# Kernel tuning notes

Measured on AMD Instinct MI355X. Metric: run time of the kernel, lower is better.

The kernel has to match this reference:

```python
import jax, jax.numpy as jnp
import numpy as np
import math

B, S, D, H, DFF = 2, 2048, 1024, 16, 4096
DK = D // H
EPS = 1e-6


def setup_inputs() -> dict:
    key = jax.random.key(0)
    ks = jax.random.split(key, 12)
    s = 0.02
    return {
        "x": jax.random.normal(ks[0], (B, S, D), jnp.float32),
        "mask": jnp.ones((B, S), jnp.int32),
        "wq": jax.random.normal(ks[1], (D, D), jnp.float32) * s,
        "bq": jnp.zeros((D,), jnp.float32),
        "wk": jax.random.normal(ks[2], (D, D), jnp.float32) * s,
        "bk": jnp.zeros((D,), jnp.float32),
        "wv": jax.random.normal(ks[3], (D, D), jnp.float32) * s,
        "bv": jnp.zeros((D,), jnp.float32),
        "wo": jax.random.normal(ks[4], (D, D), jnp.float32) * s,
        "bo": jnp.zeros((D,), jnp.float32),
        "g1": jnp.ones((D,), jnp.float32),
        "b1": jnp.zeros((D,), jnp.float32),
        "g2": jnp.ones((D,), jnp.float32),
        "b2": jnp.zeros((D,), jnp.float32),
        "w1": jax.random.normal(ks[5], (DFF, D), jnp.float32) * s,
        "bf1": jnp.zeros((DFF,), jnp.float32),
        "w2": jax.random.normal(ks[6], (D, DFF), jnp.float32) * s,
        "bf2": jnp.zeros((D,), jnp.float32),
    }


def _gelu(x):
    # x * 0.5 * (1 + erf(x / sqrt(2))) -- exact erf-based GELU as in source
    return x * 0.5 * (1.0 + jax.lax.erf(x * (1.0 / math.sqrt(2.0))))


def _layernorm(x, gamma, beta):
    # torch.std uses unbiased (ddof=1); eps is OUTSIDE the sqrt in the source
    mean = jnp.mean(x, axis=-1, keepdims=True)
    std = jnp.std(x, axis=-1, keepdims=True, ddof=1)
    return gamma * (x - mean) / (std + EPS) + beta


def _block(x, mask, wq, bq, wk, bk, wv, bv, wo, bo, g1, b1, g2, b2, w1, bf1, w2, bf2):
    # multi-head attention (dropout is identity in eval mode)
    q = (x @ wq.T + bq).reshape(B, S, H, DK).transpose(0, 2, 1, 3)  # bhsd
    k = (x @ wk.T + bk).reshape(B, S, H, DK).transpose(0, 2, 1, 3)
    v = (x @ wv.T + bv).reshape(B, S, H, DK).transpose(0, 2, 1, 3)
    scores = jnp.einsum("bhsd,bhtd->bhst", q, k) / math.sqrt(DK)
    scores = jnp.where(mask[:, None, None, :] == 0, -1e9, scores)
    attn = jax.nn.softmax(scores, axis=-1)
    cv = jnp.einsum("bhst,bhtd->bhsd", attn, v)
    cv = cv.transpose(0, 2, 1, 3).reshape(B, S, D)
    hd = cv @ wo.T + bo
    # residual + norm1
    hd = _layernorm(x + hd, g1, b1)
    # position-wise FFN with erf GELU
    ff = _gelu(hd @ w1.T + bf1) @ w2.T + bf2
    return _layernorm(hd + ff, g2, b2)


def reference(x, mask, wq, bq, wk, bk, wv, bv, wo, bo, g1, b1, g2, b2, w1, bf1, w2, bf2):
    return _block(x, mask, wq, bq, wk, bk, wv, bv, wo, bo, g1, b1, g2, b2, w1, bf1, w2, bf2)
```

## Files before the change

kernel.cpp:

```cpp
#include <hip/hip_runtime.h>
#include <hip/hip_bf16.h>

#define B_   2
#define S_   2048
#define D_   1024
#define H_   16
#define DK_  64
#define DFF_ 4096
#define M_   (B_*S_)

typedef unsigned short u16;
typedef __attribute__((ext_vector_type(8))) short short8;
typedef __attribute__((ext_vector_type(4))) short bf16x4;
typedef __attribute__((ext_vector_type(4))) float floatx4;

__device__ __forceinline__ u16 f2bf(float f) {
    union { float f; unsigned u; } v; v.f = f;
    unsigned r = v.u + 0x7fffu + ((v.u >> 16) & 1u);
    return (u16)(r >> 16);
}
__device__ __forceinline__ u16 f2bf_fast(float f) {
    __hip_bfloat16 h = __float2bfloat16(f);
    return *reinterpret_cast<u16*>(&h);
}

__device__ __forceinline__ float exp2_fast(float f) {
    return __builtin_amdgcn_exp2f(f);
}

__device__ __forceinline__ void g2l16(const u16* g, u16* l) {
    __builtin_amdgcn_global_load_lds((const __attribute__((address_space(1))) void*)g,
                                     (__attribute__((address_space(3))) void*)l,
                                     16, 0, 0);
}

__device__ __forceinline__ unsigned lds_off(const void* p) {
    return (unsigned)(unsigned long long)p;
}

#define TRB16(dst, va, IMM)                                                    \
    asm volatile("ds_read_b64_tr_b16 %0, %1 offset:" #IMM                      \
                 : "=v"(dst) : "v"(va))

__global__ __launch_bounds__(256) void cvt_all(
    const float* __restrict__ x,  const float* __restrict__ wq,
    const float* __restrict__ wk, const float* __restrict__ wv,
    const float* __restrict__ wo, const float* __restrict__ w1,
    const float* __restrict__ w2,
    u16* __restrict__ xb, u16* __restrict__ wqkvb, u16* __restrict__ wob,
    u16* __restrict__ w1b, u16* __restrict__ w2b) {
    for (int i = blockIdx.x * 256 + threadIdx.x; i < 4194304;
         i += gridDim.x * 256) {
        const float* s; u16* d; int off;
        if (i < 1048576)      { s = x;  d = xb;    off = i; }
        else if (i < 1310720) { s = wq; d = wqkvb; off = i - 1048576; }
        else if (i < 1572864) { s = wk; d = wqkvb + 1048576; off = i - 1310720; }
        else if (i < 1835008) { s = wv; d = wqkvb + 2097152; off = i - 1572864; }
        else if (i < 2097152) { s = wo; d = wob;   off = i - 1835008; }
        else if (i < 3145728) { s = w1; d = w1b;   off = i - 2097152; }
        else                  { s = w2; d = w2b;   off = i - 3145728; }
        float4 v = reinterpret_cast<const float4*>(s)[off];
        ushort4 o;
        o.x = f2bf(v.x); o.y = f2bf(v.y); o.z = f2bf(v.z); o.w = f2bf(v.w);
        reinterpret_cast<ushort4*>(d)[off] = o;
    }
}

__global__ __launch_bounds__(256) void prep_misc(const float* __restrict__ bq,
                                                 const float* __restrict__ bk,
                                                 const float* __restrict__ bv,
                                                 const int* __restrict__ mask,
                                                 float* __restrict__ bqkv,
                                                 float* __restrict__ mbias) {
    int i = blockIdx.x * 256 + threadIdx.x;
    if (i < 3 * D_) {
        float v = (i < D_) ? bq[i] : (i < 2 * D_) ? bk[i - D_] : bv[i - 2 * D_];
        bqkv[i] = v;
    } else if (i < 3 * D_ + B_ * S_) {
        int k = i - 3 * D_;
        mbias[k] = (mask[k] == 0) ? -1.44269504e9f : 0.0f;
    }
}

template <int EPI>
__global__ __launch_bounds__(512, 2) void gemm256_bt(const u16* __restrict__ A,
                                                     const u16* __restrict__ Bw,
                                                     const float* __restrict__ bias,
                                                     u16* __restrict__ Cb,
                                                     int N, int K) {
    __shared__ alignas(16) u16 sA[2][2][8192];
    __shared__ alignas(16) u16 sB[2][2][8192];
    const int tid = threadIdx.x;
    const int wid = tid >> 6, lane = tid & 63;
    const int lrow = lane & 15, lgrp = lane >> 4;
    const int wm = wid >> 2, wn = wid & 3;

    const int nbx = gridDim.x;
    const int nwg = nbx * gridDim.y;
    const int orig = blockIdx.y * nbx + blockIdx.x;
    const int qd = nwg >> 3, rr = nwg & 7, xc = orig & 7, oi = orig >> 3;
    const int swz = (xc < rr ? xc * (qd + 1) : rr * (qd + 1) + (xc - rr) * qd) + oi;
    const int m0 = (swz % nbx) * 256, n0 = (swz / nbx) * 256;

    const u16* Ab = A + (size_t)m0 * K;
    const u16* Bb = Bw + (size_t)n0 * K;
    const int T = K >> 6;

    const int c0 = (wid * 2 + 0) * 64 + lane;
    const int c1 = (wid * 2 + 1) * 64 + lane;
    const int r0 = c0 >> 3, g0 = c0 & 7;
    const int r1 = c1 >> 3, g1 = c1 & 7;
    const size_t so0 = (size_t)r0 * K + (size_t)((g0 ^ (r0 & 7)) * 8);
    const size_t so1 = (size_t)r1 * K + (size_t)((g1 ^ (r1 & 7)) * 8);
    const int d0 = (wid * 2 + 0) * 512;
    const int d1 = (wid * 2 + 1) * 512;

    auto stageA = [&](int par, int half, int kt) {
        const u16* src = Ab + (size_t)(half * 128) * K + kt * 64;
        g2l16(src + so0, &sA[par][half][d0]);
        g2l16(src + so1, &sA[par][half][d1]);
    };
    auto stageB = [&](int par, int half, int kt) {
        const u16* src = Bb + (size_t)(half * 128) * K + kt * 64;
        g2l16(src + so0, &sB[par][half][d0]);
        g2l16(src + so1, &sB[par][half][d1]);
    };

    stageA(0, 0, 0); stageA(0, 1, 0);
    stageB(0, 0, 0); stageB(0, 1, 0);
    if (T > 1) { stageB(1, 0, 1); stageB(1, 1, 1); }
    asm volatile("s_waitcnt vmcnt(4)" ::: "memory");
    asm volatile("s_barrier" ::: "memory");

    floatx4 acc[8][4] = {};
    const int rbase = (wn & 1) * 64;
    const int bhalf = wn >> 1;

    for (int t = 0; t < T; t++) {
        const int par = t & 1;
        const char* baseA = (const char*)&sA[par][wm][0];
        const char* baseB = (const char*)&sB[par][bhalf][0];
        short8 bfr[4][2];
#pragma unroll
        for (int ph = 0; ph < 4; ph++) {
            if (ph == 0) {
#pragma unroll
                for (int nj = 0; nj < 4; nj++) {
                    int rb = rbase + nj * 16 + lrow;
#pragma unroll
                    for (int kk = 0; kk < 2; kk++) {
                        int off = rb * 128 + (((kk * 4 + lgrp) ^ (lrow & 7)) * 16);
                        bfr[nj][kk] = *reinterpret_cast<const short8*>(baseB + off);
                    }
                }
            }
            short8 af[2][2];
#pragma unroll
            for (int a = 0; a < 2; a++) {
                int ra = (2 * ph + a) * 16 + lrow;
#pragma unroll
                for (int kk = 0; kk < 2; kk++) {
                    int off = ra * 128 + (((kk * 4 + lgrp) ^ (lrow & 7)) * 16);
                    af[a][kk] = *reinterpret_cast<const short8*>(baseA + off);
                }
            }
            if (ph == 0) { if (t + 1 < T) stageA(par ^ 1, 0, t + 1); }
            if (ph == 1) { if (t + 1 < T) stageA(par ^ 1, 1, t + 1); }
            if (ph == 2) { if (t + 2 < T) stageB(par, 0, t + 2); }
            if (ph == 3) { if (t + 2 < T) stageB(par, 1, t + 2); }

            asm volatile("s_barrier" ::: "memory");
            asm volatile("s_waitcnt lgkmcnt(0)" ::: "memory");
            __builtin_amdgcn_sched_barrier(0);

            __builtin_amdgcn_s_setprio(1);
#pragma unroll
            for (int a = 0; a < 2; a++)
#pragma unroll
                for (int nj = 0; nj < 4; nj++) {
                    acc[2 * ph + a][nj] = __builtin_amdgcn_mfma_f32_16x16x32_bf16(
                        af[a][0], bfr[nj][0], acc[2 * ph + a][nj], 0, 0, 0);
                    acc[2 * ph + a][nj] = __builtin_amdgcn_mfma_f32_16x16x32_bf16(
                        af[a][1], bfr[nj][1], acc[2 * ph + a][nj], 0, 0, 0);
                }
            __builtin_amdgcn_s_setprio(0);

            if (ph == 3) {
                if (t >= T - 3) asm volatile("s_waitcnt vmcnt(0)" ::: "memory");
                else            asm volatile("s_waitcnt vmcnt(4)" ::: "memory");
            }
            asm volatile("s_barrier" ::: "memory");
        }
    }

#pragma unroll
    for (int mi = 0; mi < 8; mi++) {
        int row = m0 + wm * 128 + mi * 16 + lgrp * 4;
#pragma unroll
        for (int nj = 0; nj < 4; nj++) {
            int col = n0 + wn * 64 + nj * 16 + lrow;
            float bc = bias[col];
#pragma unroll
            for (int j = 0; j < 4; j++) {
                float v = acc[mi][nj][j] + bc;
                if (EPI == 2) v = 0.5f * v * (1.0f + erff(v * 0.70710678118654752f));
                Cb[(size_t)(row + j) * N + col] = f2bf(v);
            }
        }
    }
}

template <int EPI>
__global__ __launch_bounds__(256) void gemm_bt(const u16* __restrict__ A,
                                               const u16* __restrict__ Bw,
                                               const float* __restrict__ bias,
                                               float* __restrict__ Cf,
                                               u16* __restrict__ Cb,
                                               int N, int K) {
    __shared__ u16 sA[128 * 32];
    __shared__ u16 sB[128 * 32];
    const int tid = threadIdx.x;
    const int wid = tid >> 6, lane = tid & 63;
    const int lrow = lane & 15, lgrp = lane >> 4;

    const int nbx = gridDim.x;
    const int nwg = nbx * gridDim.y;
    const int orig = blockIdx.y * nbx + blockIdx.x;
    const int qd = nwg >> 3, rr = nwg & 7, xc = orig & 7, oi = orig >> 3;
    const int swz = (xc < rr ? xc * (qd + 1) : rr * (qd + 1) + (xc - rr) * qd) + oi;
    const int m0 = (swz % nbx) * 128, n0 = (swz / nbx) * 128;

    const int wm = wid >> 1, wn = wid & 1;
    const int ar = lane >> 2, ac = lane & 3;

    floatx4 acc[4][4] = {};
    const u16* Ab = A + (size_t)m0 * K;
    const u16* Bb = Bw + (size_t)n0 * K;

    for (int k0 = 0; k0 < K; k0 += 32) {
#pragma unroll
        for (int i = 0; i < 2; i++) {
            int seg = wid * 2 + i;
            int row = seg * 16 + ar;
            g2l16(Ab + (size_t)row * K + k0 + ac * 8, &sA[seg * 512]);
            g2l16(Bb + (size_t)row * K + k0 + ac * 8, &sB[seg * 512]);
        }
        __syncthreads();
        short8 af[4], bfr[4];
#pragma unroll
        for (int mi = 0; mi < 4; mi++)
            af[mi] = *reinterpret_cast<const short8*>(
                &sA[(wm * 64 + mi * 16 + lrow) * 32 + lgrp * 8]);
#pragma unroll
        for (int ni = 0; ni < 4; ni++)
            bfr[ni] = *reinterpret_cast<const short8*>(
                &sB[(wn * 64 + ni * 16 + lrow) * 32 + lgrp * 8]);
#pragma unroll
        for (int mi = 0; mi < 4; mi++)
#pragma unroll
            for (int ni = 0; ni < 4; ni++)
                acc[mi][ni] = __builtin_amdgcn_mfma_f32_16x16x32_bf16(
                    af[mi], bfr[ni], acc[mi][ni], 0, 0, 0);
        __syncthreads();
    }

#pragma unroll
    for (int mi = 0; mi < 4; mi++) {
        int row = m0 + wm * 64 + mi * 16 + lgrp * 4;
#pragma unroll
        for (int ni = 0; ni < 4; ni++) {
            int col = n0 + wn * 64 + ni * 16 + lrow;
            float bc = bias[col];
#pragma unroll
            for (int j = 0; j < 4; j++) {
                float v = acc[mi][ni][j] + bc;
                if (EPI == 1)
                    Cf[(size_t)(row + j) * N + col] = v;
                else
                    Cb[(size_t)(row + j) * N + col] = f2bf(v);
            }
        }
    }
}

__global__ __launch_bounds__(512) void attn_kernel(const u16* __restrict__ QKV,
                                                   const float* __restrict__ mbias,
                                                   u16* __restrict__ O) {
    const int SD = 3 * D_;
    __shared__ alignas(16) u16 ktL[2][4096];
    __shared__ alignas(16) u16 vtL[2][4096];
    __shared__ alignas(16) u16 pL[8][1024];

    const int orig = blockIdx.y * gridDim.x + blockIdx.x;
    const int swz = (orig & 7) * 64 + (orig >> 3);
    const int qt = swz & 15, bh = swz >> 4;
    const int b = bh >> 4, h = bh & 15;

    const int tid = threadIdx.x, wid = tid >> 6, lane = tid & 63;
    const int lrow = lane & 15, lgrp = lane >> 4;

    const u16* Qp = QKV + h * DK_;
    const u16* Kp = QKV + D_ + h * DK_;
    const u16* Vp = QKV + 2 * D_ + h * DK_;
    const float* mbrow = mbias + b * S_;

    const int qr = qt * 128 + wid * 16 + lrow;
    const u16* qrow = Qp + (size_t)(b * S_ + qr) * SD;
    short8 aq0 = *reinterpret_cast<const short8*>(qrow + lgrp * 8);
    short8 aq1 = *reinterpret_cast<const short8*>(qrow + 32 + lgrp * 8);

    const int q8 = wid * 64 + lane;
    const int krow = q8 >> 3, kcb = q8 & 7;
    const u16* kq = Kp + (size_t)(b * S_ + krow) * SD + ((kcb ^ (krow & 7)) * 8);
    const int ov = wid * 512 + lane * 8;
    const int vk = ((ov >> 6) & 7) * 8 + ((ov >> 9) & 1) * 4 + ((ov >> 4) & 3);
    const int vd = (ov >> 10) * 16 + (ov & 8);
    const u16* vq = Vp + (size_t)(b * S_ + vk) * SD + vd;

    auto issue = [&](int bufIdx) {
        g2l16(kq, &ktL[bufIdx][wid * 512]);
        g2l16(vq, &vtL[bufIdx][wid * 512]);
        kq += 64 * SD;
        vq += 64 * SD;
    };

    floatx4 accO[4] = {};
    float mrun = -1e30f, lrun = 0.f;
    const float SC2 = 0.18033688011112042f;

    issue(0);
    int cur = 0;
    for (int t = 0; t < S_ / 64; t++) {
        const int kv0 = t * 64;
        if (t < S_ / 64 - 1) {
            issue(cur ^ 1);
            asm volatile("s_waitcnt vmcnt(2)" ::: "memory");
        } else {
            asm volatile("s_waitcnt vmcnt(0)" ::: "memory");
        }
        __builtin_amdgcn_s_barrier();
        asm volatile("" ::: "memory");

        const u16* ktc = ktL[cur];
        const unsigned vva = lds_off(vtL[cur]) + lane * 8;

        float4 mb[4];
#pragma unroll
        for (int ni = 0; ni < 4; ni++)
            mb[ni] = *reinterpret_cast<const float4*>(mbrow + kv0 + ni * 16 + lgrp * 4);

        floatx4 st[4];
        __builtin_amdgcn_s_setprio(1);
#pragma unroll
        for (int ni = 0; ni < 4; ni++) {
            int row = ni * 16 + lrow;
            int off0 = (row * 128 + lgrp * 16) ^ ((lrow & 7) << 4);
            int off1 = (row * 128 + 64 + lgrp * 16) ^ ((lrow & 7) << 4);
            short8 bk0 = *reinterpret_cast<const short8*>((const char*)ktc + off0);
            short8 bk1 = *reinterpret_cast<const short8*>((const char*)ktc + off1);
            floatx4 z = {0.f, 0.f, 0.f, 0.f};
            z = __builtin_amdgcn_mfma_f32_16x16x32_bf16(bk0, aq0, z, 0, 0, 0);
            z = __builtin_amdgcn_mfma_f32_16x16x32_bf16(bk1, aq1, z, 0, 0, 0);
            st[ni] = z;
        }
        __builtin_amdgcn_s_setprio(0);

        bf16x4 vt0[4], vt1[4], vt2[4], vt3[4];
#pragma unroll
        for (int nd = 0; nd < 4; nd++) {
            unsigned a = vva + nd * 2048;
            TRB16(vt0[nd], a, 0);
            TRB16(vt1[nd], a, 1024);
            TRB16(vt2[nd], a, 512);
            TRB16(vt3[nd], a, 1536);
        }

        float pm[4][4];
#pragma unroll
        for (int ni = 0; ni < 4; ni++) {
            const float* mbp = reinterpret_cast<const float*>(&mb[ni]);
#pragma unroll
            for (int j = 0; j < 4; j++)
                pm[ni][j] = fmaf(st[ni][j], SC2, mbp[j]);
        }
        float pmax = pm[0][0];
#pragma unroll
        for (int ni = 0; ni < 4; ni++)
#pragma unroll
            for (int j = 0; j < 4; j++) pmax = fmaxf(pmax, pm[ni][j]);
        pmax = fmaxf(pmax, __shfl_xor(pmax, 16, 64));
        pmax = fmaxf(pmax, __shfl_xor(pmax, 32, 64));

        bool upd = !__all(pmax - mrun <= 11.5f);
        float fac = 1.0f;
        if (upd) {
            float mn = fmaxf(mrun, pmax);
            fac = exp2_fast(mrun - mn);
            mrun = mn;
        }

        float p[4][4];
        float s = 0.f;
#pragma unroll
        for (int ni = 0; ni < 4; ni++)
#pragma unroll
            for (int j = 0; j < 4; j++) {
                float e = exp2_fast(pm[ni][j] - mrun);
                p[ni][j] = e;
                s += e;
            }
        s += __shfl_xor(s, 16, 64);
        s += __shfl_xor(s, 32, 64);
        lrun = lrun * fac + s;

#pragma unroll
        for (int ni = 0; ni < 4; ni++) {
            bf16x4 pw;
#pragma unroll
            for (int j = 0; j < 4; j++) pw[j] = (short)f2bf_fast(p[ni][j]);
            unsigned woff = (unsigned)((lrow * 128 + ni * 32 + lgrp * 8) ^ ((lrow & 7) << 4));
            *reinterpret_cast<bf16x4*>((char*)pL[wid] + woff) = pw;
        }

        if (upd) {
            float f0 = __shfl(fac, lgrp * 4 + 0, 64);
            float f1 = __shfl(fac, lgrp * 4 + 1, 64);
            float f2 = __shfl(fac, lgrp * 4 + 2, 64);
            float f3 = __shfl(fac, lgrp * 4 + 3, 64);
#pragma unroll
            for (int nd = 0; nd < 4; nd++) {
                floatx4 tt = accO[nd];
                tt[0] *= f0; tt[1] *= f1; tt[2] *= f2; tt[3] *= f3;
                accO[nd] = tt;
            }
        }

        asm volatile("s_waitcnt lgkmcnt(0)" ::: "memory");
        __builtin_amdgcn_sched_barrier(0);

        unsigned ra0 = (unsigned)((lrow * 128 + lgrp * 16) ^ ((lrow & 7) << 4));
        unsigned ra1 = (unsigned)((lrow * 128 + 64 + lgrp * 16) ^ ((lrow & 7) << 4));
        short8 ap0 = *reinterpret_cast<const short8*>((const char*)pL[wid] + ra0);
        short8 ap1 = *reinterpret_cast<const short8*>((const char*)pL[wid] + ra1);

        __builtin_amdgcn_s_setprio(1);
#pragma unroll
        for (int nd = 0; nd < 4; nd++) {
            short8 bv0 = __builtin_shufflevector(vt0[nd], vt1[nd], 0, 1, 2, 3, 4, 5, 6, 7);
            short8 bv1 = __builtin_shufflevector(vt2[nd], vt3[nd], 0, 1, 2, 3, 4, 5, 6, 7);
            accO[nd] = __builtin_amdgcn_mfma_f32_16x16x32_bf16(ap0, bv0, accO[nd], 0, 0, 0);
            accO[nd] = __builtin_amdgcn_mfma_f32_16x16x32_bf16(ap1, bv1, accO[nd], 0, 0, 0);
        }
        __builtin_amdgcn_s_setprio(0);

        asm volatile("" ::: "memory");
        __builtin_amdgcn_s_barrier();
        cur ^= 1;
    }

    float linv = 1.0f / lrun;
    float li[4];
#pragma unroll
    for (int j = 0; j < 4; j++) li[j] = __shfl(linv, lgrp * 4 + j, 64);
#pragma unroll
    for (int nd = 0; nd < 4; nd++)
#pragma unroll
        for (int j = 0; j < 4; j++) {
            int r = lgrp * 4 + j;
            float v = accO[nd][j] * li[j];
            O[(size_t)(b * S_ + qt * 128 + wid * 16 + r) * D_ + h * DK_ + nd * 16 + lrow] =
                f2bf_fast(v);
        }
}

__global__ __launch_bounds__(256) void ln_kernel(const float* __restrict__ X,
                                                 const float* __restrict__ R,
                                                 const float* __restrict__ gam,
                                                 const float* __restrict__ bet,
                                                 float* __restrict__ outf,
                                                 u16* __restrict__ outb) {
    __shared__ float ws1[4], ws2[4];
    const int row = blockIdx.x, tid = threadIdx.x;
    const float4 x = reinterpret_cast<const float4*>(X + (size_t)row * D_)[tid];
    const float4 r = reinterpret_cast<const float4*>(R + (size_t)row * D_)[tid];
    float4 v; v.x = x.x + r.x; v.y = x.y + r.y; v.z = x.z + r.z; v.w = x.w + r.w;

    float s = v.x + v.y + v.z + v.w;
#pragma unroll
    for (int m = 32; m >= 1; m >>= 1) s += __shfl_xor(s, m, 64);
    if ((tid & 63) == 0) ws1[tid >> 6] = s;
    __syncthreads();
    float mean = (ws1[0] + ws1[1] + ws1[2] + ws1[3]) * (1.f / D_);

    float4 d; d.x = v.x - mean; d.y = v.y - mean; d.z = v.z - mean; d.w = v.w - mean;
    float q = d.x * d.x + d.y * d.y + d.z * d.z + d.w * d.w;
#pragma unroll
    for (int m = 32; m >= 1; m >>= 1) q += __shfl_xor(q, m, 64);
    if ((tid & 63) == 0) ws2[tid >> 6] = q;
    __syncthreads();
    float var = (ws2[0] + ws2[1] + ws2[2] + ws2[3]) * (1.f / (D_ - 1));
    float inv = 1.f / (sqrtf(var) + 1e-6f);

    const float4 g = reinterpret_cast<const float4*>(gam)[tid];
    const float4 bb = reinterpret_cast<const float4*>(bet)[tid];
    float4 o;
    o.x = g.x * d.x * inv + bb.x;
    o.y = g.y * d.y * inv + bb.y;
    o.z = g.z * d.z * inv + bb.z;
    o.w = g.w * d.w * inv + bb.w;
    if (outf) reinterpret_cast<float4*>(outf + (size_t)row * D_)[tid] = o;
    if (outb) {
        ushort4 ob;
        ob.x = f2bf(o.x); ob.y = f2bf(o.y); ob.z = f2bf(o.z); ob.w = f2bf(o.w);
        reinterpret_cast<ushort4*>(outb + (size_t)row * D_)[tid] = ob;
    }
}

extern "C" void kernel_launch(void* const* d_in, const int* in_sizes, int n_in,
                              void* d_out, int out_size, void* d_ws, size_t ws_size,
                              hipStream_t stream) {
    const float* x    = (const float*)d_in[0];
    const int*   mask = (const int*)d_in[1];
    const float* wq   = (const float*)d_in[2];
    const float* bq   = (const float*)d_in[3];
    const float* wk   = (const float*)d_in[4];
    const float* bk   = (const float*)d_in[5];
    const float* wv   = (const float*)d_in[6];
    const float* bv   = (const float*)d_in[7];
    const float* wo   = (const float*)d_in[8];
    const float* bo   = (const float*)d_in[9];
    const float* g1   = (const float*)d_in[10];
    const float* b1   = (const float*)d_in[11];
    const float* g2   = (const float*)d_in[12];
    const float* b2   = (const float*)d_in[13];
    const float* w1   = (const float*)d_in[14];
    const float* bf1  = (const float*)d_in[15];
    const float* w2   = (const float*)d_in[16];
    const float* bf2  = (const float*)d_in[17];
    float* out = (float*)d_out;

    char* ws = (char*)d_ws;
    size_t off = 0;
    auto alloc = [&](size_t bytes) -> void* {
        void* p = ws + off;
        off += (bytes + 255) & ~(size_t)255;
        return p;
    };
    u16*   xb    = (u16*)  alloc((size_t)M_ * D_ * 2);
    u16*   wqkvb = (u16*)  alloc((size_t)3 * D_ * D_ * 2);
    u16*   wob   = (u16*)  alloc((size_t)D_ * D_ * 2);
    u16*   w1b   = (u16*)  alloc((size_t)DFF_ * D_ * 2);
    u16*   w2b   = (u16*)  alloc((size_t)D_ * DFF_ * 2);
    float* bqkv  = (float*)alloc((size_t)3 * D_ * 4);
    float* mbias = (float*)alloc((size_t)B_ * S_ * 4);
    u16*   qkvb  = (u16*)  alloc((size_t)M_ * 3 * D_ * 2);
    u16*   cvb   = (u16*)  alloc((size_t)M_ * D_ * 2);
    float* projf = (float*)alloc((size_t)M_ * D_ * 4);
    float* hdf   = (float*)alloc((size_t)M_ * D_ * 4);
    u16*   hdb   = (u16*)  alloc((size_t)M_ * D_ * 2);
    u16*   ff1b  = (u16*)  alloc((size_t)M_ * DFF_ * 2);
    float* ff2f  = (float*)alloc((size_t)M_ * D_ * 4);

    cvt_all<<<2048, 256, 0, stream>>>(x, wq, wk, wv, wo, w1, w2,
                                      xb, wqkvb, wob, w1b, w2b);
    prep_misc<<<28, 256, 0, stream>>>(bq, bk, bv, mask, bqkv, mbias);

    gemm256_bt<0><<<dim3(M_ / 256, 3 * D_ / 256), 512, 0, stream>>>(
        xb, wqkvb, bqkv, qkvb, 3 * D_, D_);

    attn_kernel<<<dim3(S_ / 128, B_ * H_), 512, 0, stream>>>(qkvb, mbias, cvb);

    gemm_bt<1><<<dim3(M_ / 128, D_ / 128), 256, 0, stream>>>(
        cvb, wob, bo, projf, nullptr, D_, D_);

    ln_kernel<<<M_, 256, 0, stream>>>(x, projf, g1, b1, hdf, hdb);

    gemm256_bt<2><<<dim3(M_ / 256, DFF_ / 256), 512, 0, stream>>>(
        hdb, w1b, bf1, ff1b, DFF_, D_);

    gemm_bt<1><<<dim3(M_ / 128, D_ / 128), 256, 0, stream>>>(
        ff1b, w2b, bf2, ff2f, nullptr, D_, DFF_);

    ln_kernel<<<M_, 256, 0, stream>>>(hdf, ff2f, g2, b2, out, nullptr);
}
```

Baseline: 424.4 us.

## Split-K the output and FFN2 GEMMs and reduce partials inside LayerNorm

The two GEMMs with N=1024 (attention output projection and FFN down-projection) now split the K dimension across blockIdx.z, 2-way and 4-way respectively. Each split writes its own fp32 partial result, and only the first split adds the bias. The LayerNorm kernel is templated on the number of residual inputs, so it sums the partials together with the residual. The goal is to fill the GPU better than the previous 256-block grid, which gave roughly one workgroup per CU and left the long-K loop poorly latency-hidden; the cost is extra fp32 partial traffic to and from HBM. The workspace is also reassigned to fixed offsets so the 4-way partial buffer reuses memory whose contents are no longer needed.

```diff
diff --git a/kernel.cpp b/kernel.cpp
--- a/kernel.cpp
+++ b/kernel.cpp
@@ -210,18 +210,19 @@
     }
 }
 
-template <int EPI>
-__global__ __launch_bounds__(256) void gemm_bt(const u16* __restrict__ A,
+template <int SPLIT>
+__global__ __launch_bounds__(256) void gemm_sk(const u16* __restrict__ A,
                                                const u16* __restrict__ Bw,
                                                const float* __restrict__ bias,
                                                float* __restrict__ Cf,
-                                               u16* __restrict__ Cb,
                                                int N, int K) {
     __shared__ u16 sA[128 * 32];
     __shared__ u16 sB[128 * 32];
     const int tid = threadIdx.x;
     const int wid = tid >> 6, lane = tid & 63;
     const int lrow = lane & 15, lgrp = lane >> 4;
+    const int z = blockIdx.z;
+    const int Kc = K / SPLIT;
 
     const int nbx = gridDim.x;
     const int nwg = nbx * gridDim.y;
@@ -236,8 +237,9 @@
     floatx4 acc[4][4] = {};
     const u16* Ab = A + (size_t)m0 * K;
     const u16* Bb = Bw + (size_t)n0 * K;
-
-    for (int k0 = 0; k0 < K; k0 += 32) {
+    float* Co = Cf + (size_t)z * M_ * N;
+
+    for (int k0 = z * Kc; k0 < (z + 1) * Kc; k0 += 32) {
 #pragma unroll
         for (int i = 0; i < 2; i++) {
             int seg = wid * 2 + i;
@@ -270,15 +272,10 @@
 #pragma unroll
         for (int ni = 0; ni < 4; ni++) {
             int col = n0 + wn * 64 + ni * 16 + lrow;
-            float bc = bias[col];
-#pragma unroll
-            for (int j = 0; j < 4; j++) {
-                float v = acc[mi][ni][j] + bc;
-                if (EPI == 1)
-                    Cf[(size_t)(row + j) * N + col] = v;
-                else
-                    Cb[(size_t)(row + j) * N + col] = f2bf(v);
-            }
+            float bc = (z == 0) ? bias[col] : 0.0f;
+#pragma unroll
+            for (int j = 0; j < 4; j++)
+                Co[(size_t)(row + j) * N + col] = acc[mi][ni][j] + bc;
         }
     }
 }
@@ -473,17 +470,36 @@
         }
 }
 
+template <int NR>
 __global__ __launch_bounds__(256) void ln_kernel(const float* __restrict__ X,
-                                                 const float* __restrict__ R,
+                                                 const float* __restrict__ R0,
+                                                 const float* __restrict__ R1,
+                                                 const float* __restrict__ R2,
+                                                 const float* __restrict__ R3,
                                                  const float* __restrict__ gam,
                                                  const float* __restrict__ bet,
                                                  float* __restrict__ outf,
                                                  u16* __restrict__ outb) {
     __shared__ float ws1[4], ws2[4];
     const int row = blockIdx.x, tid = threadIdx.x;
-    const float4 x = reinterpret_cast<const float4*>(X + (size_t)row * D_)[tid];
-    const float4 r = reinterpret_cast<const float4*>(R + (size_t)row * D_)[tid];
-    float4 v; v.x = x.x + r.x; v.y = x.y + r.y; v.z = x.z + r.z; v.w = x.w + r.w;
+    const size_t ro = (size_t)row * D_;
+    float4 v = reinterpret_cast<const float4*>(X + ro)[tid];
+    {
+        const float4 r = reinterpret_cast<const float4*>(R0 + ro)[tid];
+        v.x += r.x; v.y += r.y; v.z += r.z; v.w += r.w;
+    }
+    if (NR >= 2) {
+        const float4 r = reinterpret_cast<const float4*>(R1 + ro)[tid];
+        v.x += r.x; v.y += r.y; v.z += r.z; v.w += r.w;
+    }
+    if (NR >= 3) {
+        const float4 r = reinterpret_cast<const float4*>(R2 + ro)[tid];
+        v.x += r.x; v.y += r.y; v.z += r.z; v.w += r.w;
+    }
+    if (NR >= 4) {
+        const float4 r = reinterpret_cast<const float4*>(R3 + ro)[tid];
+        v.x += r.x; v.y += r.y; v.z += r.z; v.w += r.w;
+    }
 
     float s = v.x + v.y + v.z + v.w;
 #pragma unroll
@@ -508,11 +524,11 @@
     o.y = g.y * d.y * inv + bb.y;
     o.z = g.z * d.z * inv + bb.z;
     o.w = g.w * d.w * inv + bb.w;
-    if (outf) reinterpret_cast<float4*>(outf + (size_t)row * D_)[tid] = o;
+    if (outf) reinterpret_cast<float4*>(outf + ro)[tid] = o;
     if (outb) {
         ushort4 ob;
         ob.x = f2bf(o.x); ob.y = f2bf(o.y); ob.z = f2bf(o.z); ob.w = f2bf(o.w);
-        reinterpret_cast<ushort4*>(outb + (size_t)row * D_)[tid] = ob;
+        reinterpret_cast<ushort4*>(outb + ro)[tid] = ob;
     }
 }
 
@@ -540,26 +556,22 @@
     float* out = (float*)d_out;
 
     char* ws = (char*)d_ws;
-    size_t off = 0;
-    auto alloc = [&](size_t bytes) -> void* {
-        void* p = ws + off;
-        off += (bytes + 255) & ~(size_t)255;
-        return p;
-    };
-    u16*   xb    = (u16*)  alloc((size_t)M_ * D_ * 2);
-    u16*   wqkvb = (u16*)  alloc((size_t)3 * D_ * D_ * 2);
-    u16*   wob   = (u16*)  alloc((size_t)D_ * D_ * 2);
-    u16*   w1b   = (u16*)  alloc((size_t)DFF_ * D_ * 2);
-    u16*   w2b   = (u16*)  alloc((size_t)D_ * DFF_ * 2);
-    float* bqkv  = (float*)alloc((size_t)3 * D_ * 4);
-    float* mbias = (float*)alloc((size_t)B_ * S_ * 4);
-    u16*   qkvb  = (u16*)  alloc((size_t)M_ * 3 * D_ * 2);
-    u16*   cvb   = (u16*)  alloc((size_t)M_ * D_ * 2);
-    float* projf = (float*)alloc((size_t)M_ * D_ * 4);
-    float* hdf   = (float*)alloc((size_t)M_ * D_ * 4);
-    u16*   hdb   = (u16*)  alloc((size_t)M_ * D_ * 2);
-    u16*   ff1b  = (u16*)  alloc((size_t)M_ * DFF_ * 2);
-    float* ff2f  = (float*)alloc((size_t)M_ * D_ * 4);
+    const size_t MB = 1u << 20;
+    u16*   xb    = (u16*)  (ws + 0 * MB);
+    u16*   wqkvb = (u16*)  (ws + 8 * MB);
+    u16*   qkvb  = (u16*)  (ws + 14 * MB);
+    u16*   cvb   = (u16*)  (ws + 38 * MB);
+    float* p0    = (float*)(ws + 46 * MB);
+    float* p1    = (float*)(ws + 62 * MB);
+    float* qpart = (float*)(ws + 0 * MB);
+    u16*   wob   = (u16*)  (ws + 78 * MB);
+    u16*   w1b   = (u16*)  (ws + 80 * MB);
+    u16*   w2b   = (u16*)  (ws + 88 * MB);
+    float* bqkv  = (float*)(ws + 96 * MB);
+    float* mbias = (float*)(ws + 96 * MB + 65536);
+    float* hdf   = (float*)(ws + 97 * MB);
+    u16*   hdb   = (u16*)  (ws + 113 * MB);
+    u16*   ff1b  = (u16*)  (ws + 121 * MB);
 
     cvt_all<<<2048, 256, 0, stream>>>(x, wq, wk, wv, wo, w1, w2,
                                       xb, wqkvb, wob, w1b, w2b);
@@ -570,16 +582,20 @@
 
     attn_kernel<<<dim3(S_ / 128, B_ * H_), 512, 0, stream>>>(qkvb, mbias, cvb);
 
-    gemm_bt<1><<<dim3(M_ / 128, D_ / 128), 256, 0, stream>>>(
-        cvb, wob, bo, projf, nullptr, D_, D_);
-
-    ln_kernel<<<M_, 256, 0, stream>>>(x, projf, g1, b1, hdf, hdb);
+    gemm_sk<2><<<dim3(M_ / 128, D_ / 128, 2), 256, 0, stream>>>(
+        cvb, wob, bo, p0, D_, D_);
+
+    ln_kernel<2><<<M_, 256, 0, stream>>>(x, p0, p1, nullptr, nullptr,
+                                         g1, b1, hdf, hdb);
 
     gemm256_bt<2><<<dim3(M_ / 256, DFF_ / 256), 512, 0, stream>>>(
         hdb, w1b, bf1, ff1b, DFF_, D_);
 
-    gemm_bt<1><<<dim3(M_ / 128, D_ / 128), 256, 0, stream>>>(
-        ff1b, w2b, bf2, ff2f, nullptr, D_, DFF_);
-
-    ln_kernel<<<M_, 256, 0, stream>>>(hdf, ff2f, g2, b2, out, nullptr);
-}
+    gemm_sk<4><<<dim3(M_ / 128, D_ / 128, 4), 256, 0, stream>>>(
+        ff1b, w2b, bf2, qpart, D_, DFF_);
+
+    ln_kernel<4><<<M_, 256, 0, stream>>>(hdf, qpart, qpart + (size_t)M_ * D_,
+                                         qpart + 2 * (size_t)M_ * D_,
+                                         qpart + 3 * (size_t)M_ * D_,
+                                         g2, b2, out, nullptr);
+}
```

After: 410.6 us. 3.3% less time.
